# Performance work log

Measured on AMD Instinct MI355X. Metric: run time of the kernel, lower is better.

## Reference

```python
import jax, jax.numpy as jnp
import numpy as np

IN_CH, OUT_CH, HID, NHEAD = 4, 1, 256, 8
VDIM = HID // NHEAD
LOCALITIES = (2.0, 10.0, 10.0, 10.0, 10.0, 200.0)
N_BLOCKS = len(LOCALITIES) - 2
INPUT_RES, LATENT_RES, OUTPUT_RES = (64, 64), (32, 32), (64, 64)
BATCH = 8


def pairwise_dist(res1x, res1y, res2x, res2y):
    gx1 = jnp.linspace(0, 1, res1x + 1)[:-1]
    gy1 = jnp.linspace(0, 1, res1y + 1)[:-1]
    g1x, g1y = jnp.meshgrid(gx1, gy1, indexing='xy')
    grid1 = jnp.stack([g1x.flatten(), g1y.flatten()], axis=-1)
    gx2 = jnp.linspace(0, 1, res2x + 1)[:-1]
    gy2 = jnp.linspace(0, 1, res2y + 1)[:-1]
    g2x, g2y = jnp.meshgrid(gx2, gy2, indexing='xy')
    grid2 = jnp.stack([g2x.flatten(), g2y.flatten()], axis=-1)
    diff = grid1[:, None, :] - grid2[None, :, :]
    return (jnp.sum(diff ** 2, axis=-1) / 2.0).astype(jnp.float32)


def pos_att(m_dist, x, r, w, locality):
    # m_dist:[Nq,Nk]  x:[B,Nk,HID]  r:[H,1,1]  w:[H,HID,VDIM]
    scale = jnp.tan(0.25 * jnp.pi * (1 - 1e-07) * (1 + jnp.sin(r)))
    sd = m_dist[None, :, :] * scale  # [H,Nq,Nk]
    if locality <= 100:
        thr = jnp.percentile(sd, locality, axis=-1, keepdims=True)
        sd = jnp.where(sd <= thr, sd, jnp.inf)
    att = jax.nn.softmax(-sd, axis=-1)  # [H,Nq,Nk]
    value = jnp.einsum('bnj,hjk->bhnk', x, w)  # [B,H,Nk,VDIM]
    out = jnp.einsum('hjn,bhnk->bhjk', att, value)  # [B,H,Nq,VDIM]
    out = jnp.transpose(out, (0, 2, 1, 3)).reshape(x.shape[0], m_dist.shape[0], -1)
    return jax.nn.gelu(out)


def lin(x, w, b):
    # eqx.nn.Linear: w:[out,in], b:[out]
    return jnp.einsum('bni,oi->bno', x, w) + b


def setup_inputs() -> dict:
    key = jax.random.key(0)
    ks = jax.random.split(key, 20)
    Ni = INPUT_RES[0] * INPUT_RES[1]
    s_h = 1.0 / jnp.sqrt(HID)
    s_in = 1.0 / jnp.sqrt(IN_CH)
    return {
        'x': jax.random.normal(ks[0], (BATCH, Ni, IN_CH), jnp.float32),
        'en_fc1_w': jax.random.uniform(ks[1], (HID, IN_CH), jnp.float32, -s_in, s_in),
        'en_fc1_b': jax.random.uniform(ks[2], (HID,), jnp.float32, -s_in, s_in),
        'down_r': jax.random.normal(ks[3], (NHEAD, 1, 1), jnp.float32),
        'down_w': jax.random.normal(ks[4], (NHEAD, HID, VDIM), jnp.float32) * s_h,
        'pa_r': jax.random.normal(ks[5], (N_BLOCKS, NHEAD, 1, 1), jnp.float32),
        'pa_w': jax.random.normal(ks[6], (N_BLOCKS, NHEAD, HID, VDIM), jnp.float32) * s_h,
        'mlp1_w': jax.random.uniform(ks[7], (N_BLOCKS, HID, HID), jnp.float32, -s_h, s_h),
        'mlp1_b': jax.random.uniform(ks[8], (N_BLOCKS, HID), jnp.float32, -s_h, s_h),
        'mlp2_w': jax.random.uniform(ks[9], (N_BLOCKS, HID, HID), jnp.float32, -s_h, s_h),
        'mlp2_b': jax.random.uniform(ks[10], (N_BLOCKS, HID), jnp.float32, -s_h, s_h),
        'res_w': jax.random.uniform(ks[11], (N_BLOCKS, HID, HID), jnp.float32, -s_h, s_h),
        'res_b': jax.random.uniform(ks[12], (N_BLOCKS, HID), jnp.float32, -s_h, s_h),
        'up_r': jax.random.normal(ks[13], (NHEAD, 1, 1), jnp.float32),
        'up_w': jax.random.normal(ks[14], (NHEAD, HID, VDIM), jnp.float32) * s_h,
        'de_fc1_w': jax.random.uniform(ks[15], (HID, HID), jnp.float32, -s_h, s_h),
        'de_fc1_b': jax.random.uniform(ks[16], (HID,), jnp.float32, -s_h, s_h),
        'de_fc2_w': jax.random.uniform(ks[17], (OUT_CH, HID), jnp.float32, -s_h, s_h),
        'de_fc2_b': jax.random.uniform(ks[18], (OUT_CH,), jnp.float32, -s_h, s_h),
    }


def reference(x, en_fc1_w, en_fc1_b, down_r, down_w, pa_r, pa_w,
              mlp1_w, mlp1_b, mlp2_w, mlp2_b, res_w, res_b,
              up_r, up_w, de_fc1_w, de_fc1_b, de_fc2_w, de_fc2_b):
    m_dist_down = pairwise_dist(LATENT_RES[0], LATENT_RES[1], INPUT_RES[0], INPUT_RES[1])
    m_dist_proc = pairwise_dist(LATENT_RES[0], LATENT_RES[1], LATENT_RES[0], LATENT_RES[1])
    m_dist_up = pairwise_dist(OUTPUT_RES[0], OUTPUT_RES[1], LATENT_RES[0], LATENT_RES[1])

    h = jax.nn.gelu(lin(x, en_fc1_w, en_fc1_b))
    h = pos_att(m_dist_down, h, down_r, down_w, LOCALITIES[0])
    for i in range(N_BLOCKS):
        pa_out = pos_att(m_dist_proc, h, pa_r[i], pa_w[i], LOCALITIES[1 + i])
        mlp_out = lin(jax.nn.gelu(lin(pa_out, mlp1_w[i], mlp1_b[i])), mlp2_w[i], mlp2_b[i])
        residual = lin(h, res_w[i], res_b[i])
        h = jax.nn.gelu(mlp_out + residual)
    h = pos_att(m_dist_up, h, up_r, up_w, LOCALITIES[-1])
    h = jax.nn.gelu(lin(h, de_fc1_w, de_fc1_b))
    return lin(h, de_fc2_w, de_fc2_b)
```

## Files before the change

### kernel.cpp

```cpp
#include <hip/hip_runtime.h>
#include <math.h>


#define PI_F 3.14159265358979323846f

typedef __attribute__((ext_vector_type(8))) short short8;
typedef __attribute__((ext_vector_type(4))) float float4v;
typedef __attribute__((ext_vector_type(4))) unsigned short ushort4v;

__device__ __forceinline__ float gelu_f(float x) {
  float u = 0.7978845608028654f * (x + 0.044715f * x * x * x);
  float e = __expf(2.0f * u);
  float t = 1.0f - 2.0f / (e + 1.0f);
  return 0.5f * x * (1.0f + t);
}

__device__ __forceinline__ float head_scale(float r) {
  return tanf(0.25f * PI_F * (1.0f - 1e-7f) * (1.0f + sinf(r)));
}

__device__ __forceinline__ unsigned short f2bf(float f) {
  union { float f; unsigned u; } c; c.f = f;
  unsigned u = c.u + 0x7FFFu + ((c.u >> 16) & 1u);
  return (unsigned short)(u >> 16);
}
__device__ __forceinline__ float bf2f(unsigned short h) {
  union { unsigned u; float f; } c; c.u = ((unsigned)h) << 16;
  return c.f;
}
__device__ __forceinline__ void split_bf(float f, unsigned short& hi,
                                         unsigned short& lo) {
  hi = f2bf(f);
  lo = f2bf(f - bf2f(hi));
}

__global__ __launch_bounds__(256) void k_enc(
    const float* __restrict__ x, const float* __restrict__ w,
    const float* __restrict__ b, unsigned short* __restrict__ ahi,
    unsigned short* __restrict__ alo) {
  int row = blockIdx.x;
  int o = threadIdx.x;
  float4 xv = *(const float4*)(x + (size_t)row * 4);
  float4 wv = *(const float4*)(w + (size_t)o * 4);
  float s = xv.x * wv.x + xv.y * wv.y + xv.z * wv.z + xv.w * wv.w + b[o];
  s = gelu_f(s);
  unsigned short hi, lo;
  split_bf(s, hi, lo);
  ahi[(size_t)row * 256 + o] = hi;
  alo[(size_t)row * 256 + o] = lo;
}

__global__ __launch_bounds__(256) void k_split_all(
    const float* __restrict__ down_w, const float* __restrict__ de1_w,
    const float* __restrict__ up_w, const float* __restrict__ pa_w,
    const float* __restrict__ mlp1_w, const float* __restrict__ mlp2_w,
    const float* __restrict__ res_w, unsigned short* __restrict__ whi,
    unsigned short* __restrict__ wlo) {
  int i = blockIdx.x * 256 + threadIdx.x;
  float f;
  if (i < 65536) {
    int n = i >> 8, k = i & 255;
    f = down_w[(n >> 5) * 8192 + k * 32 + (n & 31)];
  } else if (i < 131072) {
    f = de1_w[i - 65536];
  } else if (i < 196608) {
    int j = i - 131072;
    int n = j >> 8, k = j & 255;
    f = up_w[(n >> 5) * 8192 + k * 32 + (n & 31)];
  } else if (i < 458752) {
    int j = i - 196608;
    int blk = j >> 16, r = j & 65535;
    int n = r >> 8, k = r & 255;
    f = pa_w[(size_t)blk * 65536 + (n >> 5) * 8192 + k * 32 + (n & 31)];
  } else if (i < 720896) {
    f = mlp1_w[i - 458752];
  } else if (i < 983040) {
    f = mlp2_w[i - 720896];
  } else {
    f = res_w[i - 983040];
  }
  unsigned short hi, lo;
  split_bf(f, hi, lo);
  whi[i] = hi;
  wlo[i] = lo;
}

template <int KRES, int CXM, int NPT, int TARGET, int TMAX>
__global__ __launch_bounds__(256) void k_thresh(int* __restrict__ thr) {
  __shared__ int wsum[4];
  int q = blockIdx.x, tid = threadIdx.x;
  int qx = q & 31, qy = q >> 5;
  int cx = qx * CXM, cy = qy * CXM;
  int d[NPT];
#pragma unroll
  for (int j = 0; j < NPT; ++j) {
    int k = tid * NPT + j;
    int kx = k & (KRES - 1), ky = k / KRES;
    int dx = cx - kx, dy = cy - ky;
    d[j] = dx * dx + dy * dy;
  }
  int lo = 0, hi = TMAX;
  while (lo < hi) {
    int mid = (lo + hi) >> 1;
    int c = 0;
#pragma unroll
    for (int j = 0; j < NPT; ++j) c += (d[j] <= mid) ? 1 : 0;
#pragma unroll
    for (int off = 32; off > 0; off >>= 1) c += __shfl_down(c, off, 64);
    if ((tid & 63) == 0) wsum[tid >> 6] = c;
    __syncthreads();
    int total = wsum[0] + wsum[1] + wsum[2] + wsum[3];
    __syncthreads();
    if (total >= TARGET) hi = mid; else lo = mid + 1;
  }
  if (tid == 0) thr[q] = lo;
}

template <int KRES, int CXM, int DSHIFT, int J2>
__global__ __launch_bounds__(256) void k_klist2(
    const float* __restrict__ rvec, const int* __restrict__ thr,
    int* __restrict__ klist2, int* __restrict__ kcnt2,
    float* __restrict__ wlist2) {
  __shared__ int cntS;
  __shared__ int sidx[J2];
  __shared__ int sdv[J2][4];
  __shared__ float denS[8][4];
  int tile = blockIdx.x, tid = threadIdx.x;
  int tx = tile & 15, ty = tile >> 4;
  int cxA[4], cyA[4], T[4];
#pragma unroll
  for (int i = 0; i < 4; ++i) {
    int qx = 2 * tx + (i & 1), qy = 2 * ty + (i >> 1);
    cxA[i] = qx * CXM; cyA[i] = qy * CXM;
    T[i] = thr[qy * 32 + qx];
  }
  if (tid == 0) cntS = 0;
  __syncthreads();
  int x0 = KRES - 1, x1 = 0, y0 = KRES - 1, y1 = 0;
#pragma unroll
  for (int i = 0; i < 4; ++i) {
    int rad = (int)sqrtf((float)T[i]);
    while ((rad + 1) * (rad + 1) <= T[i]) ++rad;
    while (rad > 0 && rad * rad > T[i]) --rad;
    x0 = min(x0, max(0, cxA[i] - rad));
    x1 = max(x1, min(KRES - 1, cxA[i] + rad));
    y0 = min(y0, max(0, cyA[i] - rad));
    y1 = max(y1, min(KRES - 1, cyA[i] + rad));
  }
  int W = x1 - x0 + 1, H = y1 - y0 + 1, tot = W * H;
  for (int p = tid; p < tot; p += 256) {
    int kx = x0 + p % W, ky = y0 + p / W;
    int d[4]; bool keep = false;
#pragma unroll
    for (int i = 0; i < 4; ++i) {
      int dx = cxA[i] - kx, dy = cyA[i] - ky;
      d[i] = dx * dx + dy * dy;
      keep = keep || (d[i] <= T[i]);
    }
    if (keep) {
      int s = atomicAdd(&cntS, 1);
      if (s < J2) {
        sidx[s] = ky * KRES + kx;
#pragma unroll
        for (int i = 0; i < 4; ++i) sdv[s][i] = d[i];
      }
    }
  }
  __syncthreads();
  int cnt = min(cntS, J2);
  int h = tid >> 5, lane = tid & 31;
  float sc = head_scale(rvec[h]) * (1.0f / (float)(1 << DSHIFT));
  float den[4] = {0.f, 0.f, 0.f, 0.f};
  for (int j = lane; j < cnt; j += 32) {
#pragma unroll
    for (int i = 0; i < 4; ++i)
      if (sdv[j][i] <= T[i]) den[i] += __expf(-sc * (float)sdv[j][i]);
  }
#pragma unroll
  for (int i = 0; i < 4; ++i) {
    float d0 = den[i];
#pragma unroll
    for (int off = 16; off > 0; off >>= 1) d0 += __shfl_down(d0, off, 32);
    if (lane == 0) denS[h][i] = d0;
  }
  __syncthreads();
  float inv[4];
#pragma unroll
  for (int i = 0; i < 4; ++i) inv[i] = 1.0f / denS[h][i];
  for (int j = lane; j < cnt; j += 32) {
    float w[4];
#pragma unroll
    for (int i = 0; i < 4; ++i)
      w[i] = (sdv[j][i] <= T[i]) ? __expf(-sc * (float)sdv[j][i]) * inv[i] : 0.f;
    float4v wv = {w[0], w[1], w[2], w[3]};
    *(float4v*)&wlist2[(((size_t)h * 256 + tile) * J2 + j) * 4] = wv;
  }
  if (tid == 0) kcnt2[tile] = cnt;
  if (h == 0)
    for (int j = lane; j < cnt; j += 32) klist2[(size_t)tile * J2 + j] = sidx[j];
}

template <int NK, int J2>
__global__ __launch_bounds__(256) void k_att3(
    const float* __restrict__ value,
    const int* __restrict__ klist2, const int* __restrict__ kcnt2,
    const float* __restrict__ wlist2, unsigned short* __restrict__ ohi,
    unsigned short* __restrict__ olo) {
  __shared__ int kls[J2];
  __shared__ float4v wls[J2];
  __shared__ float4v part[4][4][64];
  int blk = blockIdx.x;
  int tile = blk >> 3, h = blk & 7;
  int tid = threadIdx.x, g = tid & 63, s = tid >> 6;
  int cnt = kcnt2[tile];
  for (int j = tid; j < cnt; j += 256) {
    kls[j] = klist2[(size_t)tile * J2 + j];
    wls[j] = *(const float4v*)&wlist2[(((size_t)h * 256 + tile) * J2 + j) * 4];
  }
  __syncthreads();
  const float* vb = value + (size_t)h * NK * 256 + g * 4;
  float4v acc[4];
#pragma unroll
  for (int i = 0; i < 4; ++i) acc[i] = (float4v)0.0f;
  for (int j = s; j < cnt; j += 4) {
    int row = kls[j];
    float4v v = *(const float4v*)(vb + (size_t)row * 256);
    float4v w = wls[j];
    acc[0] += w.x * v;
    acc[1] += w.y * v;
    acc[2] += w.z * v;
    acc[3] += w.w * v;
  }
#pragma unroll
  for (int i = 0; i < 4; ++i) part[s][i][g] = acc[i];
  __syncthreads();
  if (tid < 64) {
    int g2 = tid;
    int ttx = tile & 15, tty = tile >> 4;
    int batch = g2 >> 3, v0 = (g2 & 7) * 4;
#pragma unroll
    for (int i = 0; i < 4; ++i) {
      float4v o4 = part[0][i][g2] + part[1][i][g2] + part[2][i][g2] +
                   part[3][i][g2];
      int q = (2 * tty + (i >> 1)) * 32 + 2 * ttx + (i & 1);
      size_t idx = ((size_t)batch * 1024 + q) * 256 + h * 32 + v0;
      ushort4v hv, lv;
#pragma unroll
      for (int c = 0; c < 4; ++c) {
        float oo = gelu_f(o4[c]);
        unsigned short hi, lo;
        split_bf(oo, hi, lo);
        hv[c] = hi; lv[c] = lo;
      }
      *(ushort4v*)(ohi + idx) = hv;
      *(ushort4v*)(olo + idx) = lv;
    }
  }
}

template <bool DUAL, int OL, bool GEL, bool OHILO>
__global__ __launch_bounds__(256) void k_mf(
    const unsigned short* __restrict__ A1hi, const unsigned short* __restrict__ A1lo,
    const unsigned short* __restrict__ W1hi, const unsigned short* __restrict__ W1lo,
    const unsigned short* __restrict__ A2hi, const unsigned short* __restrict__ A2lo,
    const unsigned short* __restrict__ W2hi, const unsigned short* __restrict__ W2lo,
    const float* __restrict__ bias, const float* __restrict__ bias2,
    float* __restrict__ outf, unsigned short* __restrict__ ohi,
    unsigned short* __restrict__ olo, int NS) {
  __shared__ unsigned short Ah[128][40], Al[128][40];
  __shared__ unsigned short Bh[128][40], Bl[128][40];
  int tid = threadIdx.x;
  int m0 = blockIdx.x * 128, n0 = blockIdx.y * 128;
  int w = tid >> 6, lane = tid & 63;
  int wm = (w >> 1) * 64, wn = (w & 1) * 64;
  int quad = lane >> 4, l16 = lane & 15;
  float4v acc[4][4];
#pragma unroll
  for (int i = 0; i < 4; ++i)
#pragma unroll
    for (int j = 0; j < 4; ++j) acc[i][j] = (float4v)0.0f;

  int srow = tid >> 1, skq = (tid & 1) * 16;
  const int KT = DUAL ? 512 : 256;
  for (int kk = 0; kk < KT; kk += 32) {
    const unsigned short *pAh, *pAl, *pWh, *pWl;
    int kb;
    if (DUAL && kk >= 256) {
      pAh = A2hi; pAl = A2lo; pWh = W2hi; pWl = W2lo; kb = kk - 256;
    } else {
      pAh = A1hi; pAl = A1lo; pWh = W1hi; pWl = W1lo; kb = kk;
    }
    {
      size_t ga = (size_t)(m0 + srow) * 256 + kb + skq;
      const uint4* pah = (const uint4*)(pAh + ga);
      const uint4* pal = (const uint4*)(pAl + ga);
      *(uint4*)&Ah[srow][skq] = pah[0];
      *(uint4*)&Ah[srow][skq + 8] = pah[1];
      *(uint4*)&Al[srow][skq] = pal[0];
      *(uint4*)&Al[srow][skq + 8] = pal[1];
      size_t gb = (size_t)(n0 + srow) * 256 + kb + skq;
      const uint4* pbh = (const uint4*)(pWh + gb);
      const uint4* pbl = (const uint4*)(pWl + gb);
      *(uint4*)&Bh[srow][skq] = pbh[0];
      *(uint4*)&Bh[srow][skq + 8] = pbh[1];
      *(uint4*)&Bl[srow][skq] = pbl[0];
      *(uint4*)&Bl[srow][skq + 8] = pbl[1];
    }
    __syncthreads();
    short8 ah[4], al[4], bh[4], bl[4];
#pragma unroll
    for (int s = 0; s < 4; ++s) {
      ah[s] = *(const short8*)&Ah[wm + s * 16 + l16][quad * 8];
      al[s] = *(const short8*)&Al[wm + s * 16 + l16][quad * 8];
      bh[s] = *(const short8*)&Bh[wn + s * 16 + l16][quad * 8];
      bl[s] = *(const short8*)&Bl[wn + s * 16 + l16][quad * 8];
    }
#pragma unroll
    for (int ms = 0; ms < 4; ++ms)
#pragma unroll
      for (int ns = 0; ns < 4; ++ns) {
        acc[ms][ns] = __builtin_amdgcn_mfma_f32_16x16x32_bf16(
            ah[ms], bh[ns], acc[ms][ns], 0, 0, 0);
        acc[ms][ns] = __builtin_amdgcn_mfma_f32_16x16x32_bf16(
            ah[ms], bl[ns], acc[ms][ns], 0, 0, 0);
        acc[ms][ns] = __builtin_amdgcn_mfma_f32_16x16x32_bf16(
            al[ms], bh[ns], acc[ms][ns], 0, 0, 0);
      }
    __syncthreads();
  }
#pragma unroll
  for (int ms = 0; ms < 4; ++ms) {
#pragma unroll
    for (int ns = 0; ns < 4; ++ns) {
      int n = n0 + wn + ns * 16 + l16;
      float bv = bias ? bias[n] : 0.0f;
      if (DUAL && bias2) bv += bias2[n];
#pragma unroll
      for (int r = 0; r < 4; ++r) {
        int m = m0 + wm + ms * 16 + quad * 4 + r;
        float c = acc[ms][ns][r] + bv;
        if (GEL) c = gelu_f(c);
        if (OHILO) {
          unsigned short chi, clo;
          split_bf(c, chi, clo);
          ohi[(size_t)m * 256 + n] = chi;
          olo[(size_t)m * 256 + n] = clo;
        } else if (OL == 0) {
          outf[(size_t)m * 256 + n] = c;
        } else {
          int N = 1 << NS;
          int bb = m >> NS, rr = m & (N - 1);
          outf[(((size_t)(n >> 5) * N + rr) * 8 + bb) * 32 + (n & 31)] = c;
        }
      }
    }
  }
}

template <bool DUAL, int OL, bool GEL, bool OHILO>
__global__ __launch_bounds__(256) void k_mf2(
    const unsigned short* __restrict__ A1hi, const unsigned short* __restrict__ A1lo,
    const unsigned short* __restrict__ W1hi, const unsigned short* __restrict__ W1lo,
    const unsigned short* __restrict__ A2hi, const unsigned short* __restrict__ A2lo,
    const unsigned short* __restrict__ W2hi, const unsigned short* __restrict__ W2lo,
    const float* __restrict__ bias, const float* __restrict__ bias2,
    float* __restrict__ outf, unsigned short* __restrict__ ohi,
    unsigned short* __restrict__ olo, int NS) {
  __shared__ unsigned short Ah[64][40], Al[64][40];
  __shared__ unsigned short Bh[64][40], Bl[64][40];
  int tid = threadIdx.x;
  int m0 = blockIdx.x * 64, n0 = blockIdx.y * 64;
  int w = tid >> 6, lane = tid & 63;
  int wm = (w >> 1) * 32, wn = (w & 1) * 32;
  int quad = lane >> 4, l16 = lane & 15;
  float4v acc[2][2];
#pragma unroll
  for (int i = 0; i < 2; ++i)
#pragma unroll
    for (int j = 0; j < 2; ++j) acc[i][j] = (float4v)0.0f;

  int srow = tid >> 2, skq = (tid & 3) * 8;
  const int KT = DUAL ? 512 : 256;
  for (int kk = 0; kk < KT; kk += 32) {
    const unsigned short *pAh, *pAl, *pWh, *pWl;
    int kb;
    if (DUAL && kk >= 256) {
      pAh = A2hi; pAl = A2lo; pWh = W2hi; pWl = W2lo; kb = kk - 256;
    } else {
      pAh = A1hi; pAl = A1lo; pWh = W1hi; pWl = W1lo; kb = kk;
    }
    {
      size_t ga = (size_t)(m0 + srow) * 256 + kb + skq;
      *(uint4*)&Ah[srow][skq] = *(const uint4*)(pAh + ga);
      *(uint4*)&Al[srow][skq] = *(const uint4*)(pAl + ga);
      size_t gb = (size_t)(n0 + srow) * 256 + kb + skq;
      *(uint4*)&Bh[srow][skq] = *(const uint4*)(pWh + gb);
      *(uint4*)&Bl[srow][skq] = *(const uint4*)(pWl + gb);
    }
    __syncthreads();
    short8 ah[2], al[2], bh[2], bl[2];
#pragma unroll
    for (int s = 0; s < 2; ++s) {
      ah[s] = *(const short8*)&Ah[wm + s * 16 + l16][quad * 8];
      al[s] = *(const short8*)&Al[wm + s * 16 + l16][quad * 8];
      bh[s] = *(const short8*)&Bh[wn + s * 16 + l16][quad * 8];
      bl[s] = *(const short8*)&Bl[wn + s * 16 + l16][quad * 8];
    }
#pragma unroll
    for (int ms = 0; ms < 2; ++ms)
#pragma unroll
      for (int ns = 0; ns < 2; ++ns) {
        acc[ms][ns] = __builtin_amdgcn_mfma_f32_16x16x32_bf16(
            ah[ms], bh[ns], acc[ms][ns], 0, 0, 0);
        acc[ms][ns] = __builtin_amdgcn_mfma_f32_16x16x32_bf16(
            ah[ms], bl[ns], acc[ms][ns], 0, 0, 0);
        acc[ms][ns] = __builtin_amdgcn_mfma_f32_16x16x32_bf16(
            al[ms], bh[ns], acc[ms][ns], 0, 0, 0);
      }
    __syncthreads();
  }
#pragma unroll
  for (int ms = 0; ms < 2; ++ms) {
#pragma unroll
    for (int ns = 0; ns < 2; ++ns) {
      int n = n0 + wn + ns * 16 + l16;
      float bv = bias ? bias[n] : 0.0f;
      if (DUAL && bias2) bv += bias2[n];
#pragma unroll
      for (int r = 0; r < 4; ++r) {
        int m = m0 + wm + ms * 16 + quad * 4 + r;
        float c = acc[ms][ns][r] + bv;
        if (GEL) c = gelu_f(c);
        if (OHILO) {
          unsigned short chi, clo;
          split_bf(c, chi, clo);
          ohi[(size_t)m * 256 + n] = chi;
          olo[(size_t)m * 256 + n] = clo;
        } else if (OL == 0) {
          outf[(size_t)m * 256 + n] = c;
        } else {
          int N = 1 << NS;
          int bb = m >> NS, rr = m & (N - 1);
          outf[(((size_t)(n >> 5) * N + rr) * 8 + bb) * 32 + (n & 31)] = c;
        }
      }
    }
  }
}

__global__ __launch_bounds__(256) void k_up_s1(
    const float* __restrict__ value,
    const float* __restrict__ rvec, float* __restrict__ T) {
  __shared__ float AxL[64][33];
  int ky = blockIdx.x, h = blockIdx.y, tid = threadIdx.x;
  float sc = head_scale(rvec[h]) * (1.0f / 8192.0f);
  float v[32];
  const float* vb = value + ((size_t)h * 1024 + ky * 32) * 256 + tid;
#pragma unroll
  for (int kx = 0; kx < 32; ++kx) v[kx] = vb[kx * 256];
  if (tid < 64) {
    int qx = tid, dxmin = qx & 1;
    for (int kx = 0; kx < 32; ++kx) {
      int dx = qx - 2 * kx;
      AxL[qx][kx] = __expf(-sc * (float)(dx * dx - dxmin));
    }
  }
  __syncthreads();
  float* tb = T + (((size_t)h * 64) * 32 + ky) * 256 + tid;
  for (int qx = 0; qx < 64; ++qx) {
    float acc = 0.f;
#pragma unroll
    for (int kx = 0; kx < 32; ++kx) acc += AxL[qx][kx] * v[kx];
    tb[(size_t)qx * 32 * 256] = acc;
  }
}

__global__ __launch_bounds__(256) void k_up_s2(
    const float* __restrict__ T, const float* __restrict__ rvec,
    unsigned short* __restrict__ ohi, unsigned short* __restrict__ olo) {
  __shared__ float AyL[64][33];
  __shared__ float Sy[64];
  __shared__ float SxS;
  int qx = blockIdx.x, h = blockIdx.y, tid = threadIdx.x;
  float sc = head_scale(rvec[h]) * (1.0f / 8192.0f);
  float t[32];
  const float* tb = T + ((size_t)h * 64 + qx) * 32 * 256 + tid;
#pragma unroll
  for (int ky = 0; ky < 32; ++ky) t[ky] = tb[ky * 256];
  if (tid < 64) {
    int qy = tid, dymin = qy & 1;
    float s = 0.f;
    for (int ky = 0; ky < 32; ++ky) {
      int dy = qy - 2 * ky;
      float e = __expf(-sc * (float)(dy * dy - dymin));
      AyL[qy][ky] = e;
      s += e;
    }
    Sy[qy] = s;
  } else if (tid >= 64 && tid < 96) {
    int kx = tid - 64, dxmin = qx & 1;
    int dx = qx - 2 * kx;
    float e = __expf(-sc * (float)(dx * dx - dxmin));
#pragma unroll
    for (int off = 16; off > 0; off >>= 1) e += __shfl_down(e, off, 32);
    if (kx == 0) SxS = e;
  }
  __syncthreads();
  float invSx = 1.0f / SxS;
  int b = tid >> 5, v = tid & 31;
  size_t base = ((size_t)b * 4096 + qx) * 256 + h * 32 + v;
  for (int qy = 0; qy < 64; ++qy) {
    float acc = 0.f;
#pragma unroll
    for (int ky = 0; ky < 32; ++ky) acc += AyL[qy][ky] * t[ky];
    float o = gelu_f(acc * invSx / Sy[qy]);
    unsigned short hi, lo;
    split_bf(o, hi, lo);
    size_t idx = base + (size_t)qy * 64 * 256;
    ohi[idx] = hi;
    olo[idx] = lo;
  }
}

__global__ __launch_bounds__(256) void k_fc2(const float* __restrict__ h,
                                             const float* __restrict__ w,
                                             const float* __restrict__ b,
                                             float* __restrict__ out) {
  int row = blockIdx.x * 4 + (threadIdx.x >> 6);
  int lane = threadIdx.x & 63;
  float4 hv = *(const float4*)(h + (size_t)row * 256 + lane * 4);
  float4 wv = *(const float4*)(w + lane * 4);
  float s = hv.x * wv.x + hv.y * wv.y + hv.z * wv.z + hv.w * wv.w;
#pragma unroll
  for (int off = 32; off > 0; off >>= 1) s += __shfl_down(s, off, 64);
  if (lane == 0) out[row] = s + b[0];
}

extern "C" void kernel_launch(void* const* d_in, const int* in_sizes, int n_in,
                              void* d_out, int out_size, void* d_ws,
                              size_t ws_size, hipStream_t stream) {
  const float* x      = (const float*)d_in[0];
  const float* en_w   = (const float*)d_in[1];
  const float* en_b   = (const float*)d_in[2];
  const float* down_r = (const float*)d_in[3];
  const float* down_w = (const float*)d_in[4];
  const float* pa_r   = (const float*)d_in[5];
  const float* pa_w   = (const float*)d_in[6];
  const float* mlp1_w = (const float*)d_in[7];
  const float* mlp1_b = (const float*)d_in[8];
  const float* mlp2_w = (const float*)d_in[9];
  const float* mlp2_b = (const float*)d_in[10];
  const float* res_w  = (const float*)d_in[11];
  const float* res_b  = (const float*)d_in[12];
  const float* up_r   = (const float*)d_in[13];
  const float* up_w   = (const float*)d_in[14];
  const float* de1_w  = (const float*)d_in[15];
  const float* de1_b  = (const float*)d_in[16];
  const float* de2_w  = (const float*)d_in[17];
  const float* de2_b  = (const float*)d_in[18];
  float* out = (float*)d_out;

  constexpr int J2 = 256;
  float* ws = (float*)d_ws;
  unsigned short* Ahi = (unsigned short*)ws;
  unsigned short* Alo = Ahi + 8388608;
  float* B = ws + 8388608;
  float* Tbuf = B + 2097152;
  unsigned short* hAhi = (unsigned short*)(ws + 16777216);
  unsigned short* hAlo = hAhi + 2097152;
  unsigned short* hBhi = hAlo + 2097152;
  unsigned short* hBlo = hBhi + 2097152;
  unsigned short* pahi = hBlo + 2097152;
  unsigned short* palo = pahi + 2097152;
  unsigned short* m1hi = palo + 2097152;
  unsigned short* m1lo = m1hi + 2097152;
  int* thrD = (int*)(ws + 25165824);
  int* thrP = thrD + 1024;
  int* cntD2 = thrP + 1024;
  int* cntP2 = cntD2 + 256;
  int* klD2 = cntP2 + 256;
  int* klP2 = klD2 + 256 * J2;
  float* wlD2 = (float*)(klP2 + 256 * J2);
  float* wlP2 = wlD2 + 2097152;
  unsigned short* Whi = (unsigned short*)(wlP2 + 2097152);
  unsigned short* Wlo = Whi + 1245184;
  const int WO_DOWN = 0, WO_DE1 = 65536, WO_UP = 131072, WO_PA = 196608,
            WO_MLP1 = 458752, WO_MLP2 = 720896, WO_RES = 983040;

  k_enc<<<32768, 256, 0, stream>>>(x, en_w, en_b, Ahi, Alo);
  k_split_all<<<4864, 256, 0, stream>>>(down_w, de1_w, up_w, pa_w, mlp1_w,
                                        mlp2_w, res_w, Whi, Wlo);
  k_thresh<64, 2, 16, 82, 7938><<<1024, 256, 0, stream>>>(thrD);
  k_thresh<32, 1, 4, 103, 1922><<<1024, 256, 0, stream>>>(thrP);
  k_klist2<64, 2, 13, J2><<<256, 256, 0, stream>>>(down_r, thrD, klD2, cntD2,
                                                   wlD2);
  k_klist2<32, 1, 11, J2><<<256, 256, 0, stream>>>(pa_r, thrP, klP2, cntP2,
                                                   wlP2);
  k_mf<false, 1, false, false><<<dim3(256, 2), 256, 0, stream>>>(
      Ahi, Alo, Whi + WO_DOWN, Wlo + WO_DOWN, nullptr, nullptr, nullptr,
      nullptr, nullptr, nullptr, B, nullptr, nullptr, 12);
  k_att3<4096, J2><<<2048, 256, 0, stream>>>(B, klD2, cntD2, wlD2, hAhi, hAlo);
  for (int i = 0; i < 4; ++i) {
    const unsigned short* hih = (i & 1) ? hBhi : hAhi;
    const unsigned short* hil = (i & 1) ? hBlo : hAlo;
    unsigned short* hoh = (i & 1) ? hAhi : hBhi;
    unsigned short* hol = (i & 1) ? hAlo : hBlo;
    k_mf2<false, 1, false, false><<<dim3(128, 4), 256, 0, stream>>>(
        hih, hil, Whi + WO_PA + i * 65536, Wlo + WO_PA + i * 65536, nullptr,
        nullptr, nullptr, nullptr, nullptr, nullptr, B, nullptr, nullptr, 10);
    k_att3<1024, J2><<<2048, 256, 0, stream>>>(B, klP2, cntP2, wlP2, pahi,
                                               palo);
    k_mf2<false, 0, true, true><<<dim3(128, 4), 256, 0, stream>>>(
        pahi, palo, Whi + WO_MLP1 + i * 65536, Wlo + WO_MLP1 + i * 65536,
        nullptr, nullptr, nullptr, nullptr, mlp1_b + i * 256, nullptr, nullptr,
        m1hi, m1lo, 0);
    k_mf2<true, 0, true, true><<<dim3(128, 4), 256, 0, stream>>>(
        m1hi, m1lo, Whi + WO_MLP2 + i * 65536, Wlo + WO_MLP2 + i * 65536, hih,
        hil, Whi + WO_RES + i * 65536, Wlo + WO_RES + i * 65536,
        mlp2_b + i * 256, res_b + i * 256, nullptr, hoh, hol, 0);
  }
  k_mf2<false, 1, false, false><<<dim3(128, 4), 256, 0, stream>>>(
      hAhi, hAlo, Whi + WO_UP, Wlo + WO_UP, nullptr, nullptr, nullptr, nullptr,
      nullptr, nullptr, B, nullptr, nullptr, 10);
  k_up_s1<<<dim3(32, 8), 256, 0, stream>>>(B, up_r, Tbuf);
  k_up_s2<<<dim3(64, 8), 256, 0, stream>>>(Tbuf, up_r, Ahi, Alo);
  k_mf<false, 0, true, false><<<dim3(256, 2), 256, 0, stream>>>(
      Ahi, Alo, Whi + WO_DE1, Wlo + WO_DE1, nullptr, nullptr, nullptr, nullptr,
      de1_b, nullptr, B, nullptr, nullptr, 0);
  k_fc2<<<8192, 256, 0, stream>>>(B, de2_w, de2_b, out);
}
```

Before: 482.3 us.

## Fuse threshold search into klist, fuse decoder fc1+fc2, split up_s1 grid

Three unrelated changes. The percentile-threshold binary search now runs inside the klist kernel for the 4 queries of each tile, which removes two launches and the threshold buffer round trip. The decoder fc1 GEMM (gelu) is fused with the fc2 dot product: a 128x128-tile MFMA kernel reduces each row's partial sums across lanes and atomically adds them into an output pre-initialised with the bias, which removes the 32 MB intermediate write and read. k_up_s1 gets a z-dimension split to double its block count. Float atomics make the output summation order nondeterministic.

```diff
diff --git a/kernel.cpp b/kernel.cpp
--- a/kernel.cpp
+++ b/kernel.cpp
@@ -85,55 +85,68 @@
   wlo[i] = lo;
 }
 
-template <int KRES, int CXM, int NPT, int TARGET, int TMAX>
-__global__ __launch_bounds__(256) void k_thresh(int* __restrict__ thr) {
-  __shared__ int wsum[4];
-  int q = blockIdx.x, tid = threadIdx.x;
-  int qx = q & 31, qy = q >> 5;
-  int cx = qx * CXM, cy = qy * CXM;
-  int d[NPT];
-#pragma unroll
-  for (int j = 0; j < NPT; ++j) {
-    int k = tid * NPT + j;
-    int kx = k & (KRES - 1), ky = k / KRES;
-    int dx = cx - kx, dy = cy - ky;
-    d[j] = dx * dx + dy * dy;
-  }
-  int lo = 0, hi = TMAX;
-  while (lo < hi) {
-    int mid = (lo + hi) >> 1;
-    int c = 0;
-#pragma unroll
-    for (int j = 0; j < NPT; ++j) c += (d[j] <= mid) ? 1 : 0;
-#pragma unroll
-    for (int off = 32; off > 0; off >>= 1) c += __shfl_down(c, off, 64);
-    if ((tid & 63) == 0) wsum[tid >> 6] = c;
-    __syncthreads();
-    int total = wsum[0] + wsum[1] + wsum[2] + wsum[3];
-    __syncthreads();
-    if (total >= TARGET) hi = mid; else lo = mid + 1;
-  }
-  if (tid == 0) thr[q] = lo;
-}
-
-template <int KRES, int CXM, int DSHIFT, int J2>
+template <int KRES, int CXM, int DSHIFT, int J2, int NPT, int TARGET,
+          int ITERS, int TMAX>
 __global__ __launch_bounds__(256) void k_klist2(
-    const float* __restrict__ rvec, const int* __restrict__ thr,
-    int* __restrict__ klist2, int* __restrict__ kcnt2,
-    float* __restrict__ wlist2) {
+    const float* __restrict__ rvec, int* __restrict__ klist2,
+    int* __restrict__ kcnt2, float* __restrict__ wlist2) {
   __shared__ int cntS;
   __shared__ int sidx[J2];
   __shared__ int sdv[J2][4];
   __shared__ float denS[8][4];
+  __shared__ int wsum4[4][4];
   int tile = blockIdx.x, tid = threadIdx.x;
   int tx = tile & 15, ty = tile >> 4;
-  int cxA[4], cyA[4], T[4];
+  int cxA[4], cyA[4];
 #pragma unroll
   for (int i = 0; i < 4; ++i) {
     int qx = 2 * tx + (i & 1), qy = 2 * ty + (i >> 1);
     cxA[i] = qx * CXM; cyA[i] = qy * CXM;
-    T[i] = thr[qy * 32 + qx];
-  }
+  }
+  int dc[4][NPT];
+#pragma unroll
+  for (int j = 0; j < NPT; ++j) {
+    int p = tid * NPT + j;
+    int kx = p & (KRES - 1), ky = p / KRES;
+#pragma unroll
+    for (int i = 0; i < 4; ++i) {
+      int dx = cxA[i] - kx, dy = cyA[i] - ky;
+      dc[i][j] = dx * dx + dy * dy;
+    }
+  }
+  int lo4[4] = {0, 0, 0, 0}, hi4[4] = {TMAX, TMAX, TMAX, TMAX};
+  for (int it = 0; it < ITERS; ++it) {
+    int mid[4], c[4] = {0, 0, 0, 0};
+#pragma unroll
+    for (int i = 0; i < 4; ++i) {
+      mid[i] = (lo4[i] + hi4[i]) >> 1;
+      if (lo4[i] < hi4[i]) {
+#pragma unroll
+        for (int j = 0; j < NPT; ++j) c[i] += (dc[i][j] <= mid[i]) ? 1 : 0;
+      }
+    }
+#pragma unroll
+    for (int i = 0; i < 4; ++i)
+#pragma unroll
+      for (int off = 32; off > 0; off >>= 1)
+        c[i] += __shfl_down(c[i], off, 64);
+    if ((tid & 63) == 0) {
+#pragma unroll
+      for (int i = 0; i < 4; ++i) wsum4[tid >> 6][i] = c[i];
+    }
+    __syncthreads();
+#pragma unroll
+    for (int i = 0; i < 4; ++i) {
+      if (lo4[i] < hi4[i]) {
+        int tot = wsum4[0][i] + wsum4[1][i] + wsum4[2][i] + wsum4[3][i];
+        if (tot >= TARGET) hi4[i] = mid[i]; else lo4[i] = mid[i] + 1;
+      }
+    }
+    __syncthreads();
+  }
+  int T[4];
+#pragma unroll
+  for (int i = 0; i < 4; ++i) T[i] = lo4[i];
   if (tid == 0) cntS = 0;
   __syncthreads();
   int x0 = KRES - 1, x1 = 0, y0 = KRES - 1, y1 = 0;
@@ -357,6 +370,92 @@
   }
 }
 
+__global__ __launch_bounds__(256) void k_mf_dec(
+    const unsigned short* __restrict__ A1hi, const unsigned short* __restrict__ A1lo,
+    const unsigned short* __restrict__ W1hi, const unsigned short* __restrict__ W1lo,
+    const float* __restrict__ b1, const float* __restrict__ w2,
+    float* __restrict__ out) {
+  __shared__ unsigned short Ah[128][40], Al[128][40];
+  __shared__ unsigned short Bh[128][40], Bl[128][40];
+  int tid = threadIdx.x;
+  int m0 = blockIdx.x * 128, n0 = blockIdx.y * 128;
+  int w = tid >> 6, lane = tid & 63;
+  int wm = (w >> 1) * 64, wn = (w & 1) * 64;
+  int quad = lane >> 4, l16 = lane & 15;
+  float4v acc[4][4];
+#pragma unroll
+  for (int i = 0; i < 4; ++i)
+#pragma unroll
+    for (int j = 0; j < 4; ++j) acc[i][j] = (float4v)0.0f;
+
+  int srow = tid >> 1, skq = (tid & 1) * 16;
+  for (int kk = 0; kk < 256; kk += 32) {
+    {
+      size_t ga = (size_t)(m0 + srow) * 256 + kk + skq;
+      const uint4* pah = (const uint4*)(A1hi + ga);
+      const uint4* pal = (const uint4*)(A1lo + ga);
+      *(uint4*)&Ah[srow][skq] = pah[0];
+      *(uint4*)&Ah[srow][skq + 8] = pah[1];
+      *(uint4*)&Al[srow][skq] = pal[0];
+      *(uint4*)&Al[srow][skq + 8] = pal[1];
+      size_t gb = (size_t)(n0 + srow) * 256 + kk + skq;
+      const uint4* pbh = (const uint4*)(W1hi + gb);
+      const uint4* pbl = (const uint4*)(W1lo + gb);
+      *(uint4*)&Bh[srow][skq] = pbh[0];
+      *(uint4*)&Bh[srow][skq + 8] = pbh[1];
+      *(uint4*)&Bl[srow][skq] = pbl[0];
+      *(uint4*)&Bl[srow][skq + 8] = pbl[1];
+    }
+    __syncthreads();
+    short8 ah[4], al[4], bh[4], bl[4];
+#pragma unroll
+    for (int s = 0; s < 4; ++s) {
+      ah[s] = *(const short8*)&Ah[wm + s * 16 + l16][quad * 8];
+      al[s] = *(const short8*)&Al[wm + s * 16 + l16][quad * 8];
+      bh[s] = *(const short8*)&Bh[wn + s * 16 + l16][quad * 8];
+      bl[s] = *(const short8*)&Bl[wn + s * 16 + l16][quad * 8];
+    }
+#pragma unroll
+    for (int ms = 0; ms < 4; ++ms)
+#pragma unroll
+      for (int ns = 0; ns < 4; ++ns) {
+        acc[ms][ns] = __builtin_amdgcn_mfma_f32_16x16x32_bf16(
+            ah[ms], bh[ns], acc[ms][ns], 0, 0, 0);
+        acc[ms][ns] = __builtin_amdgcn_mfma_f32_16x16x32_bf16(
+            ah[ms], bl[ns], acc[ms][ns], 0, 0, 0);
+        acc[ms][ns] = __builtin_amdgcn_mfma_f32_16x16x32_bf16(
+            al[ms], bh[ns], acc[ms][ns], 0, 0, 0);
+      }
+    __syncthreads();
+  }
+#pragma unroll
+  for (int ms = 0; ms < 4; ++ms) {
+#pragma unroll
+    for (int r = 0; r < 4; ++r) {
+      float p = 0.0f;
+#pragma unroll
+      for (int ns = 0; ns < 4; ++ns) {
+        int n = n0 + wn + ns * 16 + l16;
+        float c = gelu_f(acc[ms][ns][r] + b1[n]);
+        p += c * w2[n];
+      }
+      p += __shfl_xor(p, 1, 64);
+      p += __shfl_xor(p, 2, 64);
+      p += __shfl_xor(p, 4, 64);
+      p += __shfl_xor(p, 8, 64);
+      if (l16 == 0) {
+        int m = m0 + wm + ms * 16 + quad * 4 + r;
+        atomicAdd(&out[m], p);
+      }
+    }
+  }
+}
+
+__global__ __launch_bounds__(256) void k_init_out(float* __restrict__ out,
+                                                  const float* __restrict__ b) {
+  out[blockIdx.x * 256 + threadIdx.x] = b[0];
+}
+
 template <bool DUAL, int OL, bool GEL, bool OHILO>
 __global__ __launch_bounds__(256) void k_mf2(
     const unsigned short* __restrict__ A1hi, const unsigned short* __restrict__ A1lo,
@@ -451,27 +550,28 @@
 __global__ __launch_bounds__(256) void k_up_s1(
     const float* __restrict__ value,
     const float* __restrict__ rvec, float* __restrict__ T) {
-  __shared__ float AxL[64][33];
-  int ky = blockIdx.x, h = blockIdx.y, tid = threadIdx.x;
+  __shared__ float AxL[32][33];
+  int ky = blockIdx.x, h = blockIdx.y, qx0 = blockIdx.z * 32;
+  int tid = threadIdx.x;
   float sc = head_scale(rvec[h]) * (1.0f / 8192.0f);
   float v[32];
   const float* vb = value + ((size_t)h * 1024 + ky * 32) * 256 + tid;
 #pragma unroll
   for (int kx = 0; kx < 32; ++kx) v[kx] = vb[kx * 256];
-  if (tid < 64) {
-    int qx = tid, dxmin = qx & 1;
+  if (tid < 32) {
+    int qx = qx0 + tid, dxmin = qx & 1;
     for (int kx = 0; kx < 32; ++kx) {
       int dx = qx - 2 * kx;
-      AxL[qx][kx] = __expf(-sc * (float)(dx * dx - dxmin));
+      AxL[tid][kx] = __expf(-sc * (float)(dx * dx - dxmin));
     }
   }
   __syncthreads();
-  float* tb = T + (((size_t)h * 64) * 32 + ky) * 256 + tid;
-  for (int qx = 0; qx < 64; ++qx) {
+  for (int qq = 0; qq < 32; ++qq) {
+    int qx = qx0 + qq;
     float acc = 0.f;
 #pragma unroll
-    for (int kx = 0; kx < 32; ++kx) acc += AxL[qx][kx] * v[kx];
-    tb[(size_t)qx * 32 * 256] = acc;
+    for (int kx = 0; kx < 32; ++kx) acc += AxL[qq][kx] * v[kx];
+    T[(((size_t)h * 64 + qx) * 32 + ky) * 256 + tid] = acc;
   }
 }
 
@@ -520,20 +620,6 @@
     ohi[idx] = hi;
     olo[idx] = lo;
   }
-}
-
-__global__ __launch_bounds__(256) void k_fc2(const float* __restrict__ h,
-                                             const float* __restrict__ w,
-                                             const float* __restrict__ b,
-                                             float* __restrict__ out) {
-  int row = blockIdx.x * 4 + (threadIdx.x >> 6);
-  int lane = threadIdx.x & 63;
-  float4 hv = *(const float4*)(h + (size_t)row * 256 + lane * 4);
-  float4 wv = *(const float4*)(w + lane * 4);
-  float s = hv.x * wv.x + hv.y * wv.y + hv.z * wv.z + hv.w * wv.w;
-#pragma unroll
-  for (int off = 32; off > 0; off >>= 1) s += __shfl_down(s, off, 64);
-  if (lane == 0) out[row] = s + b[0];
 }
 
 extern "C" void kernel_launch(void* const* d_in, const int* in_sizes, int n_in,
@@ -574,9 +660,7 @@
   unsigned short* palo = pahi + 2097152;
   unsigned short* m1hi = palo + 2097152;
   unsigned short* m1lo = m1hi + 2097152;
-  int* thrD = (int*)(ws + 25165824);
-  int* thrP = thrD + 1024;
-  int* cntD2 = thrP + 1024;
+  int* cntD2 = (int*)(ws + 25165824);
   int* cntP2 = cntD2 + 256;
   int* klD2 = cntP2 + 256;
   int* klP2 = klD2 + 256 * J2;
@@ -590,12 +674,10 @@
   k_enc<<<32768, 256, 0, stream>>>(x, en_w, en_b, Ahi, Alo);
   k_split_all<<<4864, 256, 0, stream>>>(down_w, de1_w, up_w, pa_w, mlp1_w,
                                         mlp2_w, res_w, Whi, Wlo);
-  k_thresh<64, 2, 16, 82, 7938><<<1024, 256, 0, stream>>>(thrD);
-  k_thresh<32, 1, 4, 103, 1922><<<1024, 256, 0, stream>>>(thrP);
-  k_klist2<64, 2, 13, J2><<<256, 256, 0, stream>>>(down_r, thrD, klD2, cntD2,
-                                                   wlD2);
-  k_klist2<32, 1, 11, J2><<<256, 256, 0, stream>>>(pa_r, thrP, klP2, cntP2,
-                                                   wlP2);
+  k_klist2<64, 2, 13, J2, 16, 82, 13, 7938><<<256, 256, 0, stream>>>(
+      down_r, klD2, cntD2, wlD2);
+  k_klist2<32, 1, 11, J2, 4, 103, 11, 1922><<<256, 256, 0, stream>>>(
+      pa_r, klP2, cntP2, wlP2);
   k_mf<false, 1, false, false><<<dim3(256, 2), 256, 0, stream>>>(
       Ahi, Alo, Whi + WO_DOWN, Wlo + WO_DOWN, nullptr, nullptr, nullptr,
       nullptr, nullptr, nullptr, B, nullptr, nullptr, 12);
@@ -622,10 +704,9 @@
   k_mf2<false, 1, false, false><<<dim3(128, 4), 256, 0, stream>>>(
       hAhi, hAlo, Whi + WO_UP, Wlo + WO_UP, nullptr, nullptr, nullptr, nullptr,
       nullptr, nullptr, B, nullptr, nullptr, 10);
-  k_up_s1<<<dim3(32, 8), 256, 0, stream>>>(B, up_r, Tbuf);
+  k_up_s1<<<dim3(32, 8, 2), 256, 0, stream>>>(B, up_r, Tbuf);
   k_up_s2<<<dim3(64, 8), 256, 0, stream>>>(Tbuf, up_r, Ahi, Alo);
-  k_mf<false, 0, true, false><<<dim3(256, 2), 256, 0, stream>>>(
-      Ahi, Alo, Whi + WO_DE1, Wlo + WO_DE1, nullptr, nullptr, nullptr, nullptr,
-      de1_b, nullptr, B, nullptr, nullptr, 0);
-  k_fc2<<<8192, 256, 0, stream>>>(B, de2_w, de2_b, out);
-}
+  k_init_out<<<128, 256, 0, stream>>>(out, de2_b);
+  k_mf_dec<<<dim3(256, 2), 256, 0, stream>>>(Ahi, Alo, Whi + WO_DE1,
+                                             Wlo + WO_DE1, de1_b, de2_w, out);
+}
```

After: 493.9 us. 1.02x slower.
